# Kernel tuning notes

Measured on AMD Instinct MI355X. Metric: run time of the kernel, lower is better.

Reference implementation:

```python
import jax, jax.numpy as jnp
import numpy as np

HIDDEN = 1024
NUM_HEADS = 16
HEAD_DIM = HIDDEN // NUM_HEADS
WINDOW = 512


def setup_inputs() -> dict:
    key = jax.random.key(0)
    ks = jax.random.split(key, 6)
    b, s = 2, 4096
    x = jax.random.normal(ks[0], (b, s, HIDDEN), dtype=jnp.float32)
    attention_mask = jnp.ones((b, s), dtype=jnp.int32)
    scale = 1.0 / np.sqrt(HIDDEN)
    Wq = jax.random.normal(ks[1], (HIDDEN, HIDDEN), dtype=jnp.float32) * scale
    Wk = jax.random.normal(ks[2], (HIDDEN, HIDDEN), dtype=jnp.float32) * scale
    Wv = jax.random.normal(ks[3], (HIDDEN, HIDDEN), dtype=jnp.float32) * scale
    Wo = jax.random.normal(ks[4], (HIDDEN, HIDDEN), dtype=jnp.float32) * scale
    return {"x": x, "attention_mask": attention_mask,
            "Wq": Wq, "Wk": Wk, "Wv": Wv, "Wo": Wo}


def reference(x, attention_mask, Wq, Wk, Wv, Wo):
    b, s, d = x.shape
    # nn.Linear computes x @ W.T
    q = (x @ Wq.T).reshape(b, s, NUM_HEADS, HEAD_DIM).transpose(0, 2, 1, 3)
    k = (x @ Wk.T).reshape(b, s, NUM_HEADS, HEAD_DIM).transpose(0, 2, 1, 3)
    v = (x @ Wv.T).reshape(b, s, NUM_HEADS, HEAD_DIM).transpose(0, 2, 1, 3)
    # [b,h,s,s] scores
    scores = jnp.einsum('bhqd,bhkd->bhqk', q, k) / np.sqrt(HEAD_DIM)
    # causal sliding-window mask: allow j <= i and j >= i - window + 1
    i = jnp.arange(s)[:, None]
    j = jnp.arange(s)[None, :]
    window_mask = (j <= i) & (j >= i - WINDOW + 1)  # [s,s]
    neg_inf = jnp.finfo(scores.dtype).min
    scores = jnp.where(window_mask[None, None], scores, neg_inf)
    pad = attention_mask.astype(bool)[:, None, None, :]  # [b,1,1,s]
    scores = jnp.where(pad, scores, neg_inf)
    probs = jax.nn.softmax(scores, axis=-1)
    out = jnp.einsum('bhqk,bhkd->bhqd', probs, v)
    out = out.transpose(0, 2, 1, 3).reshape(b, s, d)
    return out @ Wo.T
```

## Files before the change

### kernel.cpp

```cpp
#include <hip/hip_runtime.h>
#include <cstdint>
#include <cstddef>

#define HID 1024
#define SEQ 4096
#define NB  2
#define NH  16
#define HD  64
#define WIN 512
#define TOK (NB*SEQ)

typedef _Float16 f16x8 __attribute__((ext_vector_type(8)));
typedef _Float16 f16x4 __attribute__((ext_vector_type(4)));
typedef float    f32x4 __attribute__((ext_vector_type(4)));

__global__ __launch_bounds__(256)
void convert_kernel(const float* __restrict__ X, const float* __restrict__ w0,
                    const float* __restrict__ w1, const float* __restrict__ w2,
                    const float* __restrict__ w3,
                    _Float16* __restrict__ Xh, _Float16* __restrict__ Wh) {
  const int bi = blockIdx.x;
  const float* src; _Float16* dst; size_t off;
  if (bi < 4096) {
    src = X; dst = Xh; off = (size_t)bi * 2048;
  } else {
    const int wi = bi - 4096, z = wi >> 9;
    src = (z == 0) ? w0 : (z == 1) ? w1 : (z == 2) ? w2 : w3;
    dst = Wh + (size_t)z * HID * HID;
    off = (size_t)(wi & 511) * 2048;
  }
  const size_t i = off + (size_t)threadIdx.x * 8;
  f32x4 a = *(const f32x4*)(src + i);
  f32x4 b = *(const f32x4*)(src + i + 4);
  f16x8 o;
#pragma unroll
  for (int r = 0; r < 4; ++r) { o[r] = (_Float16)a[r]; o[r+4] = (_Float16)b[r]; }
  *(f16x8*)(dst + i) = o;
}

__device__ __forceinline__ void gload16(const void* g, void* lds) {
  __builtin_amdgcn_global_load_lds(
      (__attribute__((address_space(1))) void*)(void*)g,
      (__attribute__((address_space(3))) void*)lds, 16, 0, 0);
}

__device__ __forceinline__ void gemm_mainloop(
    const _Float16* __restrict__ A, const _Float16* __restrict__ W,
    _Float16* sA, _Float16* sB, f32x4 (&acc)[4][4], int m0, int n0) {
  const int tid  = threadIdx.x;
  const int lane = tid & 63;
  const int wave = tid >> 6;
  const int wm = wave >> 1, wn = wave & 1;
  const int l15 = lane & 15, quad = lane >> 4;

  const int o0 = tid * 16;
  const int o1 = o0 + 4096;
  const _Float16* a0 = A + (size_t)(m0 + (o0 >> 6)) * HID + ((o0 & 63) >> 1);
  const _Float16* a1 = A + (size_t)(m0 + (o1 >> 6)) * HID + ((o1 & 63) >> 1);
  const _Float16* w0 = W + (size_t)(n0 + (o0 >> 6)) * HID + ((o0 & 63) >> 1);
  const _Float16* w1 = W + (size_t)(n0 + (o1 >> 6)) * HID + ((o1 & 63) >> 1);
  _Float16* la0 = sA + (o0 >> 1);
  _Float16* la1 = sA + (o1 >> 1);
  _Float16* lb0 = sB + (o0 >> 1);
  _Float16* lb1 = sB + (o1 >> 1);

  const int aoff = (wm*64 + l15)*32 + quad*8;
  const int boff = (wn*64 + l15)*32 + quad*8;

  for (int k0 = 0; k0 < HID; k0 += 64) {
    __syncthreads();
    gload16(a0 + k0,      la0);
    gload16(a1 + k0,      la1);
    gload16(a0 + k0 + 32, la0 + 4096);
    gload16(a1 + k0 + 32, la1 + 4096);
    gload16(w0 + k0,      lb0);
    gload16(w1 + k0,      lb1);
    gload16(w0 + k0 + 32, lb0 + 4096);
    gload16(w1 + k0 + 32, lb1 + 4096);
    __syncthreads();
#pragma unroll
    for (int s = 0; s < 2; ++s) {
      const int sb = s * 4096;
      f16x8 af[4], wf[4];
#pragma unroll
      for (int t = 0; t < 4; ++t) {
        af[t] = *(const f16x8*)(sA + sb + aoff + t*512);
        wf[t] = *(const f16x8*)(sB + sb + boff + t*512);
      }
#pragma unroll
      for (int i = 0; i < 4; ++i)
#pragma unroll
        for (int j = 0; j < 4; ++j)
          acc[i][j] = __builtin_amdgcn_mfma_f32_16x16x32_f16(af[i], wf[j], acc[i][j], 0, 0, 0);
    }
  }
}

__global__ __launch_bounds__(256, 3)
void gemm_qkv_kernel(const _Float16* __restrict__ X,
                     const _Float16* __restrict__ Wh,
                     _Float16* __restrict__ Q,
                     _Float16* __restrict__ Kb,
                     _Float16* __restrict__ Vt) {
  __shared__ __align__(16) _Float16 sA[128*64];
  __shared__ __align__(16) _Float16 sB[128*64];
  const int i  = blockIdx.x;
  const int g  = i & 7;
  const int j  = i >> 3;
  const int mi = j & 7;
  const int c  = j >> 3;
  const int z  = c >> 3;
  const int n0 = (c & 7) * 128;
  const int m0 = (g*8 + mi) * 128;
  const _Float16* W = Wh + (size_t)z * HID * HID;
  f32x4 acc[4][4] = {};
  gemm_mainloop(X, W, sA, sB, acc, m0, n0);

  const int tid  = threadIdx.x;
  const int lane = tid & 63;
  const int wave = tid >> 6;
  const int wm = wave >> 1, wn = wave & 1;
  const int l15 = lane & 15, quad = lane >> 4;

  if (z < 2) {
    _Float16* C = (z == 0) ? Q : Kb;
    const float scl = (z == 0) ? 0.125f : 1.0f;
#pragma unroll
    for (int tm = 0; tm < 4; ++tm)
#pragma unroll
      for (int tn = 0; tn < 4; ++tn) {
        const int row = m0 + wm*64 + tm*16 + quad*4;
        const int col = n0 + wn*64 + tn*16 + l15;
#pragma unroll
        for (int r = 0; r < 4; ++r)
          C[(size_t)(row + r)*HID + col] = (_Float16)(acc[tm][tn][r] * scl);
      }
  } else {
#pragma unroll
    for (int tm = 0; tm < 4; ++tm)
#pragma unroll
      for (int tn = 0; tn < 4; ++tn) {
        const int row = m0 + wm*64 + tm*16 + quad*4;
        const int col = n0 + wn*64 + tn*16 + l15;
        f16x4 v;
#pragma unroll
        for (int r = 0; r < 4; ++r) v[r] = (_Float16)acc[tm][tn][r];
        *(f16x4*)(Vt + (size_t)col*TOK + row) = v;
      }
  }
}

__global__ __launch_bounds__(256, 3)
void gemm_o_kernel(const _Float16* __restrict__ A,
                   const _Float16* __restrict__ Wo,
                   float* __restrict__ C) {
  __shared__ __align__(16) _Float16 sA[128*64];
  __shared__ __align__(16) _Float16 sB[128*64];
  const int i  = blockIdx.x;
  const int g  = i & 7;
  const int j  = i >> 3;
  const int mi = j & 7;
  const int n0 = (j >> 3) * 128;
  const int m0 = (g*8 + mi) * 128;
  f32x4 acc[4][4] = {};
  gemm_mainloop(A, Wo, sA, sB, acc, m0, n0);

  const int tid  = threadIdx.x;
  const int lane = tid & 63;
  const int wave = tid >> 6;
  const int wm = wave >> 1, wn = wave & 1;
  const int l15 = lane & 15, quad = lane >> 4;
#pragma unroll
  for (int tm = 0; tm < 4; ++tm)
#pragma unroll
    for (int tn = 0; tn < 4; ++tn) {
      const int row = m0 + wm*64 + tm*16 + quad*4;
      const int col = n0 + wn*64 + tn*16 + l15;
#pragma unroll
      for (int r = 0; r < 4; ++r)
        C[(size_t)(row + r)*HID + col] = acc[tm][tn][r];
    }
}

__global__ __launch_bounds__(512, 4)
void attn_kernel(const _Float16* __restrict__ Q, const _Float16* __restrict__ Kb,
                 const _Float16* __restrict__ Vt, const int* __restrict__ AM,
                 _Float16* __restrict__ O) {
  __shared__ __align__(16) _Float16 sK[64*64];
  __shared__ __align__(16) _Float16 sV[64*64];
  __shared__ __align__(16) _Float16 sP[8*32*64];
  __shared__ int sOK;

  const int bi = blockIdx.x;
  const int g  = bi & 7;
  const int jj = bi >> 3;
  const int combo = g*4 + (jj >> 4);
  const int h = combo & 15, b = combo >> 4;
  const int qb = jj & 15;

  const int tid  = threadIdx.x;
  const int lane = tid & 63, wave = tid >> 6;
  const int l15 = lane & 15, quad = lane >> 4;

  const int q0 = qb * 256;
  const int qw = q0 + wave * 32;

  const int swz = l15 & 7;
  const int cA8 = ((quad ^ swz) << 3);
  const int cB8 = (((quad + 4) ^ swz) << 3);

  f16x8 qf[2][2];
#pragma unroll
  for (int ns = 0; ns < 2; ++ns) {
    const size_t qbse = (size_t)(b*SEQ + qw + ns*16 + l15)*HID + h*HD + quad*8;
    qf[ns][0] = *(const f16x8*)(Q + qbse);
    qf[ns][1] = *(const f16x8*)(Q + qbse + 32);
  }

  const int kt_hi = qb*4 + 3;
  int kt_lo = qb*4 - 8; if (kt_lo < 0) kt_lo = 0;

  if (tid == 0) sOK = 1;
  __syncthreads();
  {
    int ok = 1;
    const int jbeg = kt_lo*64, jend = (kt_hi + 1)*64;
    for (int j = jbeg + tid; j < jend; j += 512) ok &= (AM[b*SEQ + j] != 0);
    if (!ok) sOK = 0;
  }
  __syncthreads();
  const bool allok = (sOK != 0);

  const int prow = tid >> 3;
  const int pc   = tid & 7;
  const int pco  = ((pc ^ (prow & 7)) << 3);
  f16x8 pk, pv;
  {
    const int j0 = kt_lo * 64;
    pk = *(const f16x8*)(Kb + (size_t)(b*SEQ + j0 + prow)*HID + h*HD + pco);
    pv = *(const f16x8*)(Vt + (size_t)(h*HD + prow)*TOK + b*SEQ + j0 + pco);
  }

  float m_run[2] = {-1e20f, -1e20f}, l_run[2] = {0.0f, 0.0f};
  f32x4 o[4][2] = {};
  _Float16* myP = sP + wave * (32*64);

  for (int kt = kt_lo; kt <= kt_hi; ++kt) {
    const int j0 = kt * 64;
    __syncthreads();
    *(f16x8*)(sK + tid*8) = pk;
    *(f16x8*)(sV + tid*8) = pv;
    __syncthreads();
    if (kt < kt_hi) {
      const int jn = (kt + 1) * 64;
      pk = *(const f16x8*)(Kb + (size_t)(b*SEQ + jn + prow)*HID + h*HD + pco);
      pv = *(const f16x8*)(Vt + (size_t)(h*HD + prow)*TOK + b*SEQ + jn + pco);
    }

    if (j0 > qw + 31 || j0 + 63 < qw - (WIN - 1)) continue;

    f32x4 sc[4][2] = {};
#pragma unroll
    for (int t = 0; t < 4; ++t) {
      const f16x8 kf0 = *(const f16x8*)(sK + (t*16 + l15)*64 + cA8);
      const f16x8 kf1 = *(const f16x8*)(sK + (t*16 + l15)*64 + cB8);
      sc[t][0] = __builtin_amdgcn_mfma_f32_16x16x32_f16(kf0, qf[0][0], sc[t][0], 0, 0, 0);
      sc[t][0] = __builtin_amdgcn_mfma_f32_16x16x32_f16(kf1, qf[0][1], sc[t][0], 0, 0, 0);
      sc[t][1] = __builtin_amdgcn_mfma_f32_16x16x32_f16(kf0, qf[1][0], sc[t][1], 0, 0, 0);
      sc[t][1] = __builtin_amdgcn_mfma_f32_16x16x32_f16(kf1, qf[1][1], sc[t][1], 0, 0, 0);
    }

    if (!allok) {
#pragma unroll
      for (int t = 0; t < 4; ++t)
#pragma unroll
        for (int r = 0; r < 4; ++r) {
          const float ad = (AM[b*SEQ + j0 + t*16 + quad*4 + r] == 0) ? -2e30f : 0.0f;
          sc[t][0][r] += ad;
          sc[t][1][r] += ad;
        }
    }

#pragma unroll
    for (int ns = 0; ns < 2; ++ns) {
      const int i = qw + ns*16 + l15;
      float mx = -1e30f;
#pragma unroll
      for (int t = 0; t < 4; ++t)
#pragma unroll
        for (int r = 0; r < 4; ++r) {
          const int j = j0 + t*16 + quad*4 + r;
          const bool valid = (unsigned)(i - j) < WIN;
          const float s = valid ? sc[t][ns][r] : -1e30f;
          sc[t][ns][r] = s;
          mx = fmaxf(mx, s);
        }
      mx = fmaxf(mx, __shfl_xor(mx, 16, 64));
      mx = fmaxf(mx, __shfl_xor(mx, 32, 64));
      const float mnew = fmaxf(m_run[ns], mx);
      const float alpha = __expf(m_run[ns] - mnew);
      m_run[ns] = mnew;
      float sum = 0.0f;
#pragma unroll
      for (int t = 0; t < 4; ++t) {
        f16x4 pvv;
#pragma unroll
        for (int r = 0; r < 4; ++r) {
          const float p = __expf(sc[t][ns][r] - mnew);
          sum += p;
          pvv[r] = (_Float16)p;
        }
        const int paddr = (ns*16 + l15)*64 + (((2*t + (quad >> 1)) ^ swz) << 3) + (quad & 1)*4;
        *(f16x4*)(myP + paddr) = pvv;
      }
      sum += __shfl_xor(sum, 16, 64);
      sum += __shfl_xor(sum, 32, 64);
      l_run[ns] = l_run[ns]*alpha + sum;
#pragma unroll
      for (int dt = 0; dt < 4; ++dt)
#pragma unroll
        for (int r = 0; r < 4; ++r) o[dt][ns][r] *= alpha;
    }

    const f16x8 pf00 = *(const f16x8*)(myP + l15*64 + cA8);
    const f16x8 pf01 = *(const f16x8*)(myP + l15*64 + cB8);
    const f16x8 pf10 = *(const f16x8*)(myP + (16 + l15)*64 + cA8);
    const f16x8 pf11 = *(const f16x8*)(myP + (16 + l15)*64 + cB8);
#pragma unroll
    for (int dt = 0; dt < 4; ++dt) {
      const f16x8 vf0 = *(const f16x8*)(sV + (dt*16 + l15)*64 + cA8);
      const f16x8 vf1 = *(const f16x8*)(sV + (dt*16 + l15)*64 + cB8);
      o[dt][0] = __builtin_amdgcn_mfma_f32_16x16x32_f16(vf0, pf00, o[dt][0], 0, 0, 0);
      o[dt][0] = __builtin_amdgcn_mfma_f32_16x16x32_f16(vf1, pf01, o[dt][0], 0, 0, 0);
      o[dt][1] = __builtin_amdgcn_mfma_f32_16x16x32_f16(vf0, pf10, o[dt][1], 0, 0, 0);
      o[dt][1] = __builtin_amdgcn_mfma_f32_16x16x32_f16(vf1, pf11, o[dt][1], 0, 0, 0);
    }
  }

  const float inv[2] = {1.0f / fmaxf(l_run[0], 1e-30f), 1.0f / fmaxf(l_run[1], 1e-30f)};
#pragma unroll
  for (int ns = 0; ns < 2; ++ns) {
    const size_t ob = (size_t)(b*SEQ + qw + ns*16 + l15)*HID + h*HD + quad*4;
#pragma unroll
    for (int dt = 0; dt < 4; ++dt) {
      f16x4 v;
#pragma unroll
      for (int r = 0; r < 4; ++r) v[r] = (_Float16)(o[dt][ns][r] * inv[ns]);
      *(f16x4*)(O + ob + dt*16) = v;
    }
  }
}

extern "C" void kernel_launch(void* const* d_in, const int* in_sizes, int n_in,
                              void* d_out, int out_size, void* d_ws, size_t ws_size,
                              hipStream_t stream) {
  const float* X  = (const float*)d_in[0];
  const int*   AM = (const int*)d_in[1];
  const float* Wq = (const float*)d_in[2];
  const float* Wk = (const float*)d_in[3];
  const float* Wv = (const float*)d_in[4];
  const float* Wo = (const float*)d_in[5];
  float* out = (float*)d_out;

  _Float16* Xh = (_Float16*)d_ws;
  _Float16* Wh = Xh + (size_t)TOK*HID;
  _Float16* Qb = Wh + (size_t)4*HID*HID;
  _Float16* Kb = Qb + (size_t)TOK*HID;
  _Float16* Vt = Kb + (size_t)TOK*HID;
  _Float16* AO = Vt + (size_t)TOK*HID;

  convert_kernel<<<dim3(4096 + 4*512), dim3(256), 0, stream>>>(X, Wq, Wk, Wv, Wo, Xh, Wh);
  gemm_qkv_kernel<<<dim3(1536), dim3(256), 0, stream>>>(Xh, Wh, Qb, Kb, Vt);
  attn_kernel<<<dim3(512), dim3(512), 0, stream>>>(Qb, Kb, Vt, AM, AO);
  gemm_o_kernel<<<dim3(512), dim3(256), 0, stream>>>(AO, Wh + (size_t)3*HID*HID, out);
}
```

Baseline: 243.9 us.

## Stage 128-key K/V tiles, use exp2 softmax, skip masking on interior tiles

The attention loop now loads K/V in 128-key stages, processed as two 64-key subtiles, which halves the number of block-wide barriers and shared-memory handoffs. The Q projection folds log2(e) into its scale so softmax can use the hardware exp2 directly instead of __expf. Tiles fully inside the sliding window skip the per-element window-mask compare. Shared memory per block grows, which could affect occupancy at 4 blocks per CU.

```diff
diff --git a/kernel.cpp b/kernel.cpp
--- a/kernel.cpp
+++ b/kernel.cpp
@@ -124,7 +124,7 @@
 
   if (z < 2) {
     _Float16* C = (z == 0) ? Q : Kb;
-    const float scl = (z == 0) ? 0.125f : 1.0f;
+    const float scl = (z == 0) ? 0.18033688011f : 1.0f;
 #pragma unroll
     for (int tm = 0; tm < 4; ++tm)
 #pragma unroll
@@ -186,8 +186,8 @@
 void attn_kernel(const _Float16* __restrict__ Q, const _Float16* __restrict__ Kb,
                  const _Float16* __restrict__ Vt, const int* __restrict__ AM,
                  _Float16* __restrict__ O) {
-  __shared__ __align__(16) _Float16 sK[64*64];
-  __shared__ __align__(16) _Float16 sV[64*64];
+  __shared__ __align__(16) _Float16 sK[128*64];
+  __shared__ __align__(16) _Float16 sV[64*128];
   __shared__ __align__(16) _Float16 sP[8*32*64];
   __shared__ int sOK;
 
@@ -217,15 +217,15 @@
     qf[ns][1] = *(const f16x8*)(Q + qbse + 32);
   }
 
-  const int kt_hi = qb*4 + 3;
-  int kt_lo = qb*4 - 8; if (kt_lo < 0) kt_lo = 0;
+  int stage_lo = (q0 - (WIN - 1));
+  stage_lo = (stage_lo < 0) ? 0 : (stage_lo & ~127);
+  const int nst = (q0 + 256 - stage_lo) >> 7;
 
   if (tid == 0) sOK = 1;
   __syncthreads();
   {
     int ok = 1;
-    const int jbeg = kt_lo*64, jend = (kt_hi + 1)*64;
-    for (int j = jbeg + tid; j < jend; j += 512) ok &= (AM[b*SEQ + j] != 0);
+    for (int j = stage_lo + tid; j < q0 + 256; j += 512) ok &= (AM[b*SEQ + j] != 0);
     if (!ok) sOK = 0;
   }
   __syncthreads();
@@ -234,106 +234,127 @@
   const int prow = tid >> 3;
   const int pc   = tid & 7;
   const int pco  = ((pc ^ (prow & 7)) << 3);
-  f16x8 pk, pv;
+  f16x8 pk0, pk1, pv0, pv1;
   {
-    const int j0 = kt_lo * 64;
-    pk = *(const f16x8*)(Kb + (size_t)(b*SEQ + j0 + prow)*HID + h*HD + pco);
-    pv = *(const f16x8*)(Vt + (size_t)(h*HD + prow)*TOK + b*SEQ + j0 + pco);
+    const _Float16* kp = Kb + (size_t)(b*SEQ + stage_lo + prow)*HID + h*HD + pco;
+    pk0 = *(const f16x8*)kp;
+    pk1 = *(const f16x8*)(kp + (size_t)64*HID);
+    const _Float16* vp = Vt + (size_t)(h*HD + prow)*TOK + b*SEQ + stage_lo + pco;
+    pv0 = *(const f16x8*)vp;
+    pv1 = *(const f16x8*)(vp + 64);
   }
 
   float m_run[2] = {-1e20f, -1e20f}, l_run[2] = {0.0f, 0.0f};
   f32x4 o[4][2] = {};
   _Float16* myP = sP + wave * (32*64);
 
-  for (int kt = kt_lo; kt <= kt_hi; ++kt) {
-    const int j0 = kt * 64;
+  for (int st = 0; st < nst; ++st) {
+    const int j0st = stage_lo + st*128;
     __syncthreads();
-    *(f16x8*)(sK + tid*8) = pk;
-    *(f16x8*)(sV + tid*8) = pv;
+    *(f16x8*)(sK + prow*64 + pc*8)        = pk0;
+    *(f16x8*)(sK + (64 + prow)*64 + pc*8) = pk1;
+    *(f16x8*)(sV + prow*128 + pc*8)       = pv0;
+    *(f16x8*)(sV + prow*128 + 64 + pc*8)  = pv1;
     __syncthreads();
-    if (kt < kt_hi) {
-      const int jn = (kt + 1) * 64;
-      pk = *(const f16x8*)(Kb + (size_t)(b*SEQ + jn + prow)*HID + h*HD + pco);
-      pv = *(const f16x8*)(Vt + (size_t)(h*HD + prow)*TOK + b*SEQ + jn + pco);
-    }
-
-    if (j0 > qw + 31 || j0 + 63 < qw - (WIN - 1)) continue;
-
-    f32x4 sc[4][2] = {};
-#pragma unroll
-    for (int t = 0; t < 4; ++t) {
-      const f16x8 kf0 = *(const f16x8*)(sK + (t*16 + l15)*64 + cA8);
-      const f16x8 kf1 = *(const f16x8*)(sK + (t*16 + l15)*64 + cB8);
-      sc[t][0] = __builtin_amdgcn_mfma_f32_16x16x32_f16(kf0, qf[0][0], sc[t][0], 0, 0, 0);
-      sc[t][0] = __builtin_amdgcn_mfma_f32_16x16x32_f16(kf1, qf[0][1], sc[t][0], 0, 0, 0);
-      sc[t][1] = __builtin_amdgcn_mfma_f32_16x16x32_f16(kf0, qf[1][0], sc[t][1], 0, 0, 0);
-      sc[t][1] = __builtin_amdgcn_mfma_f32_16x16x32_f16(kf1, qf[1][1], sc[t][1], 0, 0, 0);
-    }
-
-    if (!allok) {
-#pragma unroll
-      for (int t = 0; t < 4; ++t)
-#pragma unroll
-        for (int r = 0; r < 4; ++r) {
-          const float ad = (AM[b*SEQ + j0 + t*16 + quad*4 + r] == 0) ? -2e30f : 0.0f;
-          sc[t][0][r] += ad;
-          sc[t][1][r] += ad;
+    if (st + 1 < nst) {
+      const int jn = j0st + 128;
+      const _Float16* kp = Kb + (size_t)(b*SEQ + jn + prow)*HID + h*HD + pco;
+      pk0 = *(const f16x8*)kp;
+      pk1 = *(const f16x8*)(kp + (size_t)64*HID);
+      const _Float16* vp = Vt + (size_t)(h*HD + prow)*TOK + b*SEQ + jn + pco;
+      pv0 = *(const f16x8*)vp;
+      pv1 = *(const f16x8*)(vp + 64);
+    }
+
+#pragma unroll
+    for (int s = 0; s < 2; ++s) {
+      const int j0 = j0st + s*64;
+      if (j0 > qw + 31 || j0 + 63 < qw - (WIN - 1)) continue;
+      const bool interior = (j0 + 63 <= qw) && (j0 >= qw - (WIN - 32));
+
+      f32x4 sc[4][2] = {};
+#pragma unroll
+      for (int t = 0; t < 4; ++t) {
+        const f16x8 kf0 = *(const f16x8*)(sK + (s*64 + t*16 + l15)*64 + cA8);
+        const f16x8 kf1 = *(const f16x8*)(sK + (s*64 + t*16 + l15)*64 + cB8);
+        sc[t][0] = __builtin_amdgcn_mfma_f32_16x16x32_f16(kf0, qf[0][0], sc[t][0], 0, 0, 0);
+        sc[t][0] = __builtin_amdgcn_mfma_f32_16x16x32_f16(kf1, qf[0][1], sc[t][0], 0, 0, 0);
+        sc[t][1] = __builtin_amdgcn_mfma_f32_16x16x32_f16(kf0, qf[1][0], sc[t][1], 0, 0, 0);
+        sc[t][1] = __builtin_amdgcn_mfma_f32_16x16x32_f16(kf1, qf[1][1], sc[t][1], 0, 0, 0);
+      }
+
+      if (!allok) {
+#pragma unroll
+        for (int t = 0; t < 4; ++t)
+#pragma unroll
+          for (int r = 0; r < 4; ++r) {
+            const float ad = (AM[b*SEQ + j0 + t*16 + quad*4 + r] == 0) ? -2e30f : 0.0f;
+            sc[t][0][r] += ad;
+            sc[t][1][r] += ad;
+          }
+      }
+
+#pragma unroll
+      for (int ns = 0; ns < 2; ++ns) {
+        const int i = qw + ns*16 + l15;
+        float mx = -1e30f;
+        if (interior) {
+#pragma unroll
+          for (int t = 0; t < 4; ++t)
+#pragma unroll
+            for (int r = 0; r < 4; ++r) mx = fmaxf(mx, sc[t][ns][r]);
+        } else {
+#pragma unroll
+          for (int t = 0; t < 4; ++t)
+#pragma unroll
+            for (int r = 0; r < 4; ++r) {
+              const int j = j0 + t*16 + quad*4 + r;
+              const bool valid = (unsigned)(i - j) < WIN;
+              const float sv = valid ? sc[t][ns][r] : -1e30f;
+              sc[t][ns][r] = sv;
+              mx = fmaxf(mx, sv);
+            }
         }
-    }
-
-#pragma unroll
-    for (int ns = 0; ns < 2; ++ns) {
-      const int i = qw + ns*16 + l15;
-      float mx = -1e30f;
-#pragma unroll
-      for (int t = 0; t < 4; ++t)
-#pragma unroll
-        for (int r = 0; r < 4; ++r) {
-          const int j = j0 + t*16 + quad*4 + r;
-          const bool valid = (unsigned)(i - j) < WIN;
-          const float s = valid ? sc[t][ns][r] : -1e30f;
-          sc[t][ns][r] = s;
-          mx = fmaxf(mx, s);
+        mx = fmaxf(mx, __shfl_xor(mx, 16, 64));
+        mx = fmaxf(mx, __shfl_xor(mx, 32, 64));
+        const float mnew = fmaxf(m_run[ns], mx);
+        const float alpha = __builtin_amdgcn_exp2f(m_run[ns] - mnew);
+        m_run[ns] = mnew;
+        float sum = 0.0f;
+#pragma unroll
+        for (int t = 0; t < 4; ++t) {
+          f16x4 pvv;
+#pragma unroll
+          for (int r = 0; r < 4; ++r) {
+            const float p = __builtin_amdgcn_exp2f(sc[t][ns][r] - mnew);
+            sum += p;
+            pvv[r] = (_Float16)p;
+          }
+          const int paddr = (ns*16 + l15)*64 + (((2*t + (quad >> 1)) ^ swz) << 3) + (quad & 1)*4;
+          *(f16x4*)(myP + paddr) = pvv;
         }
-      mx = fmaxf(mx, __shfl_xor(mx, 16, 64));
-      mx = fmaxf(mx, __shfl_xor(mx, 32, 64));
-      const float mnew = fmaxf(m_run[ns], mx);
-      const float alpha = __expf(m_run[ns] - mnew);
-      m_run[ns] = mnew;
-      float sum = 0.0f;
-#pragma unroll
-      for (int t = 0; t < 4; ++t) {
-        f16x4 pvv;
-#pragma unroll
-        for (int r = 0; r < 4; ++r) {
-          const float p = __expf(sc[t][ns][r] - mnew);
-          sum += p;
-          pvv[r] = (_Float16)p;
-        }
-        const int paddr = (ns*16 + l15)*64 + (((2*t + (quad >> 1)) ^ swz) << 3) + (quad & 1)*4;
-        *(f16x4*)(myP + paddr) = pvv;
-      }
-      sum += __shfl_xor(sum, 16, 64);
-      sum += __shfl_xor(sum, 32, 64);
-      l_run[ns] = l_run[ns]*alpha + sum;
-#pragma unroll
-      for (int dt = 0; dt < 4; ++dt)
-#pragma unroll
-        for (int r = 0; r < 4; ++r) o[dt][ns][r] *= alpha;
-    }
-
-    const f16x8 pf00 = *(const f16x8*)(myP + l15*64 + cA8);
-    const f16x8 pf01 = *(const f16x8*)(myP + l15*64 + cB8);
-    const f16x8 pf10 = *(const f16x8*)(myP + (16 + l15)*64 + cA8);
-    const f16x8 pf11 = *(const f16x8*)(myP + (16 + l15)*64 + cB8);
-#pragma unroll
-    for (int dt = 0; dt < 4; ++dt) {
-      const f16x8 vf0 = *(const f16x8*)(sV + (dt*16 + l15)*64 + cA8);
-      const f16x8 vf1 = *(const f16x8*)(sV + (dt*16 + l15)*64 + cB8);
-      o[dt][0] = __builtin_amdgcn_mfma_f32_16x16x32_f16(vf0, pf00, o[dt][0], 0, 0, 0);
-      o[dt][0] = __builtin_amdgcn_mfma_f32_16x16x32_f16(vf1, pf01, o[dt][0], 0, 0, 0);
-      o[dt][1] = __builtin_amdgcn_mfma_f32_16x16x32_f16(vf0, pf10, o[dt][1], 0, 0, 0);
-      o[dt][1] = __builtin_amdgcn_mfma_f32_16x16x32_f16(vf1, pf11, o[dt][1], 0, 0, 0);
+        sum += __shfl_xor(sum, 16, 64);
+        sum += __shfl_xor(sum, 32, 64);
+        l_run[ns] = l_run[ns]*alpha + sum;
+#pragma unroll
+        for (int dt = 0; dt < 4; ++dt)
+#pragma unroll
+          for (int r = 0; r < 4; ++r) o[dt][ns][r] *= alpha;
+      }
+
+      const f16x8 pf00 = *(const f16x8*)(myP + l15*64 + cA8);
+      const f16x8 pf01 = *(const f16x8*)(myP + l15*64 + cB8);
+      const f16x8 pf10 = *(const f16x8*)(myP + (16 + l15)*64 + cA8);
+      const f16x8 pf11 = *(const f16x8*)(myP + (16 + l15)*64 + cB8);
+#pragma unroll
+      for (int dt = 0; dt < 4; ++dt) {
+        const f16x8 vf0 = *(const f16x8*)(sV + (dt*16 + l15)*128 + s*64 + cA8);
+        const f16x8 vf1 = *(const f16x8*)(sV + (dt*16 + l15)*128 + s*64 + cB8);
+        o[dt][0] = __builtin_amdgcn_mfma_f32_16x16x32_f16(vf0, pf00, o[dt][0], 0, 0, 0);
+        o[dt][0] = __builtin_amdgcn_mfma_f32_16x16x32_f16(vf1, pf01, o[dt][0], 0, 0, 0);
+        o[dt][1] = __builtin_amdgcn_mfma_f32_16x16x32_f16(vf0, pf10, o[dt][1], 0, 0, 0);
+        o[dt][1] = __builtin_amdgcn_mfma_f32_16x16x32_f16(vf1, pf11, o[dt][1], 0, 0, 0);
+      }
     }
   }
 
```

Result: faster. 238.0 us (-2.4%).
